# Kernel tuning notes

Measured on AMD Instinct MI355X. Metric: run time of the kernel, lower is better.

The kernel has to match this reference:

```python
import jax, jax.numpy as jnp
import numpy as np

B, N, FEAT, D = 8, 2048, 64, 6
RADIUS, NSAMPLE, TOPK, NHEAD, NLAYER = 0.3, 64, 16, 8, 2
EPS = 1e-5


def _bn(x, p, axis=1):
    # eval-mode batchnorm; p rows = (gamma, beta, running_mean, running_var)
    g, b, m, v = p
    sh = [1] * x.ndim
    sh[axis] = -1
    rs = lambda t: t.reshape(sh)
    return (x - rs(m)) * (rs(g) / jnp.sqrt(rs(v) + EPS)) + rs(b)


def _ln(x, g, b):
    mu = jnp.mean(x, -1, keepdims=True)
    var = jnp.mean((x - mu) ** 2, -1, keepdims=True)
    return (x - mu) / jnp.sqrt(var + EPS) * g + b


def _mha(x, w_in, b_in, w_out, b_out):
    bsz, n, e = x.shape
    hd = e // NHEAD
    qkv = x @ w_in.T + b_in                      # [B,N,3E]
    q, k, v = jnp.split(qkv, 3, axis=-1)
    sp = lambda t: t.reshape(bsz, n, NHEAD, hd).transpose(0, 2, 1, 3)  # [B,H,N,hd]
    q, k, v = sp(q), sp(k), sp(v)
    att = jax.nn.softmax(jnp.einsum('bhnd,bhmd->bhnm', q, k) * (1.0 / hd ** 0.5), axis=-1)
    o = jnp.einsum('bhnm,bhmd->bhnd', att, v).transpose(0, 2, 1, 3).reshape(bsz, n, e)
    return o @ w_out.T + b_out


def _forward(sortvec, input, tl_win, tl_bin, tl_wout, tl_bout, tl_w1, tl_b1, tl_w2, tl_b2,
             tl_ln1g, tl_ln1b, tl_ln2g, tl_ln2b,
             fg_w0, fg_b0, fg_w1, fg_b1, fg_w2, fg_b2, fbn0, fbn1, fbn2,
             rc_w0, rc_b0, rc_w1, rc_b1, rc_w2, rc_b2, rbn0, rbn1, rbn2,
             fl_w0, fl_b0, fl_w1, fl_b1, lbn0, lbn1):
    b = sortvec.shape[0]
    n = sortvec.shape[-1]
    relu = jax.nn.relu

    # --- input self-attention (2 post-norm TransformerEncoder layers) ---
    x = sortvec[:, 0].transpose(0, 2, 1)         # [B,N,FEAT]
    for l in range(NLAYER):
        a = _mha(x, tl_win[l], tl_bin[l], tl_wout[l], tl_bout[l])
        x = _ln(x + a, tl_ln1g[l], tl_ln1b[l])
        f = relu(x @ tl_w1[l].T + tl_b1[l]) @ tl_w2[l].T + tl_b2[l]
        x = _ln(x + f, tl_ln2g[l], tl_ln2b[l])

    # --- feat_generator (RFFNet: Conv2d(FEAT,1) then 1x1 convs) + BN + relu ---
    s = jnp.einsum('cf,bnf->bcn', fg_w0, x) + fg_b0[:, None]   # [B,64,N]
    s = relu(_bn(s, fbn0))
    s = relu(_bn(jnp.einsum('co,bon->bcn', fg_w1, s) + fg_b1[:, None], fbn1))
    s = relu(_bn(jnp.einsum('co,bon->bcn', fg_w2, s) + fg_b2[:, None], fbn2))
    scores = s[:, 0]                              # [B,N]

    # --- top-k point selection ---
    _, idx = jax.lax.top_k(scores, TOPK)          # [B,K]
    all_points = input.transpose(0, 2, 1)         # [B,N,6]
    bidx = jnp.arange(b)[:, None]
    query = all_points[bidx, idx]                 # [B,K,6]

    # --- query_ball_point (PointNet++ style) ---
    xyz, qxyz = all_points[..., :3], query[..., :3]
    sqr = jnp.sum((qxyz[:, :, None, :] - xyz[:, None, :, :]) ** 2, -1)   # [B,K,N]
    gidx = jnp.where(sqr > RADIUS ** 2, n, jnp.arange(n)[None, None, :])
    gidx = jnp.sort(gidx, axis=-1)[..., :NSAMPLE]                        # [B,K,S]
    gidx = jnp.where(gidx == n, gidx[..., :1], gidx)
    radius_points = all_points[jnp.arange(b)[:, None, None], gidx]       # [B,K,S,6]
    grouped = jnp.concatenate([query[:, :, None, :], radius_points], axis=2)  # [B,K,S+1,6]

    # --- radius_cnn (Conv3d (1,S+1,6) then 1x1x1) + BN3d + relu ---
    r = jnp.einsum('cpd,bkpd->bck', rc_w0, grouped) + rc_b0[:, None]     # [B,128,K]
    r = relu(_bn(r, rbn0))
    r = relu(_bn(jnp.einsum('co,bok->bck', rc_w1, r) + rc_b1[:, None], rbn1))
    r = relu(_bn(jnp.einsum('co,bok->bck', rc_w2, r) + rc_b2[:, None], rbn2))  # [B,512,K]

    # --- flatten + Linear/BN1d/relu chain ---
    h = r.reshape(b, -1)                          # [B, 512*K]
    h = relu(_bn(h @ fl_w0.T + fl_b0, lbn0))
    h = relu(_bn(h @ fl_w1.T + fl_b1, lbn1))
    return h[..., None], idx                      # [B,512,1], [B,K]


def setup_inputs() -> dict:
    key = jax.random.key(0)
    ks = iter(jax.random.split(key, 80))
    rnd = lambda shape, s=0.02: jax.random.normal(next(ks), shape, jnp.float32) * s

    def bn_p(c):
        g = 1.0 + rnd((c,))
        bb = rnd((c,))
        m = rnd((c,))
        v = 1.0 + 0.1 * jnp.abs(rnd((c,), 1.0))
        return jnp.stack([g, bb, m, v])

    F = FEAT
    return dict(
        sortvec=jax.random.normal(next(ks), (B, 1, F, N), jnp.float32),
        input=jax.random.normal(next(ks), (B, D, N), jnp.float32),
        tl_win=rnd((NLAYER, 3 * F, F)), tl_bin=rnd((NLAYER, 3 * F)),
        tl_wout=rnd((NLAYER, F, F)), tl_bout=rnd((NLAYER, F)),
        tl_w1=rnd((NLAYER, 2048, F)), tl_b1=rnd((NLAYER, 2048)),
        tl_w2=rnd((NLAYER, F, 2048)), tl_b2=rnd((NLAYER, F)),
        tl_ln1g=jnp.ones((NLAYER, F)), tl_ln1b=jnp.zeros((NLAYER, F)),
        tl_ln2g=jnp.ones((NLAYER, F)), tl_ln2b=jnp.zeros((NLAYER, F)),
        fg_w0=rnd((64, F), 0.1), fg_b0=jnp.zeros((64,)),
        fg_w1=rnd((16, 64), 0.1), fg_b1=jnp.zeros((16,)),
        fg_w2=rnd((1, 16), 0.1), fg_b2=jnp.zeros((1,)),
        fbn0=bn_p(64), fbn1=bn_p(16), fbn2=bn_p(1),
        rc_w0=rnd((128, NSAMPLE + 1, D), 0.05), rc_b0=jnp.zeros((128,)),
        rc_w1=rnd((256, 128), 0.05), rc_b1=jnp.zeros((256,)),
        rc_w2=rnd((512, 256), 0.05), rc_b2=jnp.zeros((512,)),
        rbn0=bn_p(128), rbn1=bn_p(256), rbn2=bn_p(512),
        fl_w0=rnd((1024, 512 * TOPK), 0.02), fl_b0=jnp.zeros((1024,)),
        fl_w1=rnd((512, 1024), 0.02), fl_b1=jnp.zeros((512,)),
        lbn0=bn_p(1024), lbn1=bn_p(512),
    )


def reference(sortvec, input, tl_win, tl_bin, tl_wout, tl_bout, tl_w1, tl_b1, tl_w2, tl_b2,
              tl_ln1g, tl_ln1b, tl_ln2g, tl_ln2b,
              fg_w0, fg_b0, fg_w1, fg_b1, fg_w2, fg_b2, fbn0, fbn1, fbn2,
              rc_w0, rc_b0, rc_w1, rc_b1, rc_w2, rc_b2, rbn0, rbn1, rbn2,
              fl_w0, fl_b0, fl_w1, fl_b1, lbn0, lbn1):
    return _forward(sortvec, input, tl_win, tl_bin, tl_wout, tl_bout, tl_w1, tl_b1, tl_w2, tl_b2,
                    tl_ln1g, tl_ln1b, tl_ln2g, tl_ln2b,
                    fg_w0, fg_b0, fg_w1, fg_b1, fg_w2, fg_b2, fbn0, fbn1, fbn2,
                    rc_w0, rc_b0, rc_w1, rc_b1, rc_w2, rc_b2, rbn0, rbn1, rbn2,
                    fl_w0, fl_b0, fl_w1, fl_b1, lbn0, lbn1)
```

## Files before the change

kernel.cpp:

```cpp
#include <hip/hip_runtime.h>
#include <hip/hip_bf16.h>
#include <math.h>

#define BB 8
#define NN 2048
#define FF 64
#define DD 6
#define NSAMP 64
#define TOPK 16
#define NHEAD 8
#define HD 8
#define NLAYER 2
#define EPSF 1e-5f
#define R2 0.09f

typedef short short8 __attribute__((ext_vector_type(8)));
typedef float f32x4 __attribute__((ext_vector_type(4)));
typedef unsigned uint4v __attribute__((ext_vector_type(4)));
typedef unsigned int u32;

__device__ inline unsigned pk2(float x) {
  unsigned b = __float_as_uint(x);
  unsigned hi = (b + 0x7fffu + ((b >> 16) & 1u)) >> 16;
  float r = x - __uint_as_float(hi << 16);
  unsigned c = __float_as_uint(r);
  unsigned lo = (c + 0x7fffu + ((c >> 16) & 1u)) >> 16;
  return (hi << 16) | lo;
}

__device__ inline unsigned short bf16r(float x) {
  unsigned b = __float_as_uint(x);
  return (unsigned short)((b + 0x7fffu + ((b >> 16) & 1u)) >> 16);
}

__device__ __forceinline__ void gl16(const void* g, void* l) {
  __builtin_amdgcn_global_load_lds((const __attribute__((address_space(1))) u32*)g,
                                   (__attribute__((address_space(3))) u32*)l, 16, 0, 0);
}

__global__ void k_transpose(const float* __restrict__ sv, float* __restrict__ x) {
  int i = blockIdx.x * 256 + threadIdx.x;
  if (i >= BB * NN * FF) return;
  int f = i % FF;
  int n = (i / FF) % NN;
  int b = i / (FF * NN);
  x[i] = sv[(b * FF + f) * NN + n];
}

__global__ void k_wimg(const float* __restrict__ w1, const float* __restrict__ w2,
                       unsigned short* __restrict__ img) {
  int i = blockIdx.x * 256 + threadIdx.x;
  int e = i & 4095;
  int plane = (i >> 12) & 3;
  int chg = (i >> 14) & 31;
  int l = i >> 19;
  int r = e >> 6, sh = (e >> 3) & 7, inner = e & 7;
  int s = sh ^ (r & 7);
  float v;
  if (plane < 2) v = w1[((size_t)(l * 2048 + chg * 64 + r)) * 64 + s * 8 + inner];
  else           v = w2[((size_t)(l * 64 + r)) * 2048 + chg * 64 + s * 8 + inner];
  unsigned p = pk2(v);
  img[i] = (unsigned short)((plane & 1) ? (p & 0xffffu) : (p >> 16));
}

__global__ void k_qkv3(const float* __restrict__ x, const float* __restrict__ win,
                       const float* __restrict__ bin, float* __restrict__ qbuf,
                       uint4* __restrict__ kp4, uint4* __restrict__ vp4) {
  __shared__ float xs[64 * 68];
  __shared__ float ws[64 * 68];
  int row0 = blockIdx.x * 64, y = blockIdx.y, col0 = y * 64;
  int t = threadIdx.x;
  #pragma unroll
  for (int i = 0; i < 4; ++i) {
    int q = t + i * 256, r = q >> 4, c = (q & 15) * 4;
    *(float4*)(xs + r * 68 + c) = *(const float4*)(x + (size_t)(row0 + r) * 64 + c);
    *(float4*)(ws + r * 68 + c) = *(const float4*)(win + (size_t)(col0 + r) * 64 + c);
  }
  __syncthreads();
  int tx = t & 15, ty = t >> 4;
  float acc[4][4] = {};
  for (int f = 0; f < 64; f += 4) {
    float4 xv[4], wv[4];
    #pragma unroll
    for (int ri = 0; ri < 4; ++ri) xv[ri] = *(const float4*)(xs + (ty * 4 + ri) * 68 + f);
    #pragma unroll
    for (int ci = 0; ci < 4; ++ci) wv[ci] = *(const float4*)(ws + (tx + 16 * ci) * 68 + f);
    #pragma unroll
    for (int ri = 0; ri < 4; ++ri)
      #pragma unroll
      for (int ci = 0; ci < 4; ++ci)
        acc[ri][ci] += xv[ri].x * wv[ci].x + xv[ri].y * wv[ci].y +
                       xv[ri].z * wv[ci].z + xv[ri].w * wv[ci].w;
  }
  int b = row0 >> 11, n0 = row0 & (NN - 1);
  if (y == 0) {
    #pragma unroll
    for (int ri = 0; ri < 4; ++ri)
      #pragma unroll
      for (int ci = 0; ci < 4; ++ci) {
        int r = row0 + ty * 4 + ri, c = tx + 16 * ci;
        qbuf[(size_t)r * 64 + c] = acc[ri][ci] + bin[c];
      }
    return;
  }
  __syncthreads();
  unsigned short* l16 = (unsigned short*)xs;
  if (y == 1) {
    #pragma unroll
    for (int ri = 0; ri < 4; ++ri)
      #pragma unroll
      for (int ci = 0; ci < 4; ++ci) {
        int r = ty * 4 + ri, c = tx + 16 * ci;
        l16[r * 72 + c] = bf16r(acc[ri][ci] + bin[64 + c]);
      }
    __syncthreads();
    #pragma unroll
    for (int i = 0; i < 2; ++i) {
      int idx = t + i * 256;
      int h = idx >> 6, tok = idx & 63;
      uint4 v = *(const uint4*)(l16 + tok * 72 + h * 8);
      kp4[(size_t)(b * NHEAD + h) * NN + n0 + tok] = v;
    }
  } else {
    #pragma unroll
    for (int ri = 0; ri < 4; ++ri)
      #pragma unroll
      for (int ci = 0; ci < 4; ++ci) {
        int r = ty * 4 + ri, c = tx + 16 * ci;
        l16[c * 72 + r] = bf16r(acc[ri][ci] + bin[128 + c]);
      }
    __syncthreads();
    #pragma unroll
    for (int i = 0; i < 2; ++i) {
      int idx = t + i * 256;
      int c = idx >> 3, seg = idx & 7;
      uint4 v = *(const uint4*)(l16 + c * 72 + seg * 8);
      vp4[(size_t)(b * 64 + c) * (NN / 8) + (n0 >> 3) + seg] = v;
    }
  }
}

__global__ void __launch_bounds__(256, 8)
k_attn8(const float* __restrict__ q, const uint4* __restrict__ kp4,
        const unsigned* __restrict__ vp32, float* __restrict__ a) {
  __shared__ uint4 kb4[256];
  __shared__ __attribute__((aligned(16))) unsigned short vb16[9 * 264];
  int t = threadIdx.x;
  int lane = t & 63, w = t >> 6;
  int nIdx = lane & 15, lq = lane >> 4;
  int h = blockIdx.y, b = blockIdx.z;
  int qwb = blockIdx.x * 64 + w * 16;
  int bh = b * NHEAD + h;
  const float kf = 0.35355339059327373f * 1.4426950408889634f;
  short8 qF = {0, 0, 0, 0, 0, 0, 0, 0};
  if (lq == 0) {
    const float* qr = q + ((size_t)(b * NN + qwb + nIdx)) * 64 + h * HD;
    #pragma unroll
    for (int j = 0; j < 8; ++j) qF[j] = (short)bf16r(qr[j] * kf);
  }
  f32x4 acc = {0.f, 0.f, 0.f, 0.f};
  const uint4* kbase = kp4 + (size_t)bh * NN;
  const unsigned* vbase = vp32 + (size_t)bh * HD * (NN / 2);
  int vn = nIdx < 9 ? nIdx : 8;
  int voff = ((lq & 1) << 4) + ((lq >> 1) << 3);
  if (t < 132) ((unsigned*)(vb16 + 8 * 264))[t] = 0x3f803f80u;
  uint4 kreg = kbase[t];
  unsigned vreg[4];
  #pragma unroll
  for (int i = 0; i < 4; ++i) {
    int g = t + i * 256;
    vreg[i] = vbase[(g >> 7) * (NN / 2) + (g & 127)];
  }
  for (int kc = 0; kc < NN; kc += 256) {
    __syncthreads();
    kb4[t] = kreg;
    #pragma unroll
    for (int i = 0; i < 4; ++i) {
      int g = t + i * 256;
      ((unsigned*)vb16)[(g >> 7) * 132 + (g & 127)] = vreg[i];
    }
    __syncthreads();
    if (kc + 256 < NN) {
      kreg = kbase[kc + 256 + t];
      #pragma unroll
      for (int i = 0; i < 4; ++i) {
        int g = t + i * 256;
        vreg[i] = vbase[(g >> 7) * (NN / 2) + ((kc + 256) >> 1) + (g & 127)];
      }
    }
    for (int s = 0; s < 8; ++s) {
      int kb = s * 32;
      unsigned pk_[4];
      #pragma unroll
      for (int half = 0; half < 2; ++half) {
        int key = kb + half * 16 + nIdx;
        short8 aK = {0, 0, 0, 0, 0, 0, 0, 0};
        if (lq == 0) aK = *(const short8*)(kb4 + key);
        f32x4 c = {0.f, 0.f, 0.f, 0.f};
        c = __builtin_amdgcn_mfma_f32_16x16x32_bf16(aK, qF, c, 0, 0, 0);
        unsigned u0 = __float_as_uint(__builtin_amdgcn_exp2f(c[0]));
        unsigned u1 = __float_as_uint(__builtin_amdgcn_exp2f(c[1]));
        unsigned u2 = __float_as_uint(__builtin_amdgcn_exp2f(c[2]));
        unsigned u3 = __float_as_uint(__builtin_amdgcn_exp2f(c[3]));
        pk_[half * 2]     = (u0 >> 16) | (u1 & 0xffff0000u);
        pk_[half * 2 + 1] = (u2 >> 16) | (u3 & 0xffff0000u);
      }
      unsigned e0 = (unsigned)__shfl_xor((int)pk_[0], 16);
      unsigned e1 = (unsigned)__shfl_xor((int)pk_[1], 16);
      unsigned e2 = (unsigned)__shfl_xor((int)pk_[2], 16);
      unsigned e3 = (unsigned)__shfl_xor((int)pk_[3], 16);
      bool odd = (lq & 1);
      uint4v bw;
      bw[0] = odd ? e2 : pk_[0];
      bw[1] = odd ? e3 : pk_[1];
      bw[2] = odd ? pk_[2] : e0;
      bw[3] = odd ? pk_[3] : e1;
      short8 bP = *(short8*)&bw;
      short8 aV = *(const short8*)(vb16 + vn * 264 + kb + voff);
      acc = __builtin_amdgcn_mfma_f32_16x16x32_bf16(aV, bP, acc, 0, 0, 0);
    }
  }
  float lr = __shfl(acc[0], 32 + nIdx);
  if (lq < 2) {
    int row = qwb + nIdx;
    float4 o;
    o.x = acc[0] / lr; o.y = acc[1] / lr; o.z = acc[2] / lr; o.w = acc[3] / lr;
    *(float4*)(a + ((size_t)(b * NN + row)) * 64 + h * HD + lq * 4) = o;
  }
}

__global__ void k_proj2(const float* __restrict__ a, const float* __restrict__ wout,
                        const float* __restrict__ bout, const float* __restrict__ g,
                        const float* __restrict__ be, float* __restrict__ x) {
  __shared__ float xs[64 * 68];
  __shared__ float ws[64 * 68];
  int row0 = blockIdx.x * 64;
  int t = threadIdx.x;
  #pragma unroll
  for (int i = 0; i < 4; ++i) {
    int q = t + i * 256, r = q >> 4, c = (q & 15) * 4;
    *(float4*)(xs + r * 68 + c) = *(const float4*)(a + (size_t)(row0 + r) * 64 + c);
    *(float4*)(ws + r * 68 + c) = *(const float4*)(wout + r * 64 + c);
  }
  __syncthreads();
  int tx = t & 15, ty = t >> 4;
  float acc[4][4] = {};
  for (int f = 0; f < 64; f += 4) {
    float4 xv[4], wv[4];
    #pragma unroll
    for (int ri = 0; ri < 4; ++ri) xv[ri] = *(const float4*)(xs + (ty * 4 + ri) * 68 + f);
    #pragma unroll
    for (int ci = 0; ci < 4; ++ci) wv[ci] = *(const float4*)(ws + (tx + 16 * ci) * 68 + f);
    #pragma unroll
    for (int ri = 0; ri < 4; ++ri)
      #pragma unroll
      for (int ci = 0; ci < 4; ++ci)
        acc[ri][ci] += xv[ri].x * wv[ci].x + xv[ri].y * wv[ci].y +
                       xv[ri].z * wv[ci].z + xv[ri].w * wv[ci].w;
  }
  #pragma unroll
  for (int ri = 0; ri < 4; ++ri) {
    int rl = ty * 4 + ri;
    float val[4], s = 0.f, sq = 0.f;
    #pragma unroll
    for (int ci = 0; ci < 4; ++ci) {
      int c = tx + 16 * ci;
      val[ci] = x[(size_t)(row0 + rl) * 64 + c] + bout[c] + acc[ri][ci];
      s += val[ci]; sq += val[ci] * val[ci];
    }
    #pragma unroll
    for (int off = 1; off < 16; off <<= 1) { s += __shfl_xor(s, off); sq += __shfl_xor(sq, off); }
    float mean = s * (1.f / 64.f);
    float var = sq * (1.f / 64.f) - mean * mean;
    float rstd = rsqrtf(var + EPSF);
    #pragma unroll
    for (int ci = 0; ci < 4; ++ci) {
      int c = tx + 16 * ci;
      x[(size_t)(row0 + rl) * 64 + c] = (val[ci] - mean) * rstd * g[c] + be[c];
    }
  }
}

__global__ void __launch_bounds__(256, 2)
k_ffn7(const float* __restrict__ x, const char* __restrict__ img,
       const float* __restrict__ b1, float* __restrict__ part) {
  __shared__ __attribute__((aligned(16))) char W1b[2][16384];
  __shared__ __attribute__((aligned(16))) char W2b[16384];
  __shared__ __attribute__((aligned(16))) unsigned short hpl[2][128 * 64];
  int row0 = blockIdx.x * 128;
  int ks = blockIdx.y, kc = ks * 512;
  int t = threadIdx.x, lane = t & 63, wv = t >> 6;
  int lm = lane & 15, lq = lane >> 4;
  const char* ibase = img + (size_t)ks * 8 * 32768;

  short8 axh[2][2], axl[2][2];
  #pragma unroll
  for (int m = 0; m < 2; ++m)
    #pragma unroll
    for (int kbi = 0; kbi < 2; ++kbi) {
      const float* xr = x + (size_t)(row0 + m * 64 + wv * 16 + lm) * 64 + kbi * 32 + lq * 8;
      #pragma unroll
      for (int j = 0; j < 8; ++j) {
        unsigned p = pk2(xr[j]);
        axh[m][kbi][j] = (short)(p >> 16);
        axl[m][kbi][j] = (short)(p & 0xffffu);
      }
    }
  float bv[8][4];
  #pragma unroll
  for (int ch = 0; ch < 8; ++ch)
    #pragma unroll
    for (int tn = 0; tn < 4; ++tn)
      bv[ch][tn] = b1[kc + ch * 64 + tn * 16 + lm];
  asm volatile("s_waitcnt vmcnt(0)" ::: "memory");
  __builtin_amdgcn_sched_barrier(0);
  #pragma unroll
  for (int i = 0; i < 4; ++i)
    gl16(ibase + i * 4096 + t * 16, &W1b[0][i * 4096 + t * 16]);

  f32x4 acc[2][4];
  #pragma unroll
  for (int m = 0; m < 2; ++m)
    #pragma unroll
    for (int tn = 0; tn < 4; ++tn) acc[m][tn] = (f32x4){0.f, 0.f, 0.f, 0.f};

  #pragma unroll
  for (int ch = 0; ch < 8; ++ch) {
    const int p = ch & 1;
    const char* cbase = ibase + ch * 32768;
    #pragma unroll
    for (int i = 0; i < 4; ++i)
      gl16(cbase + 16384 + i * 4096 + t * 16, &W2b[i * 4096 + t * 16]);
    if (ch < 7) {
      #pragma unroll
      for (int i = 0; i < 4; ++i)
        gl16(cbase + 32768 + i * 4096 + t * 16, &W1b[p ^ 1][i * 4096 + t * 16]);
    }
    if (ch < 7) { asm volatile("s_waitcnt vmcnt(8)" ::: "memory"); }
    else        { asm volatile("s_waitcnt vmcnt(4)" ::: "memory"); }
    __builtin_amdgcn_sched_barrier(0);
    __builtin_amdgcn_s_barrier();
    __builtin_amdgcn_sched_barrier(0);
    const char* P0h = W1b[p];
    const char* P0l = W1b[p] + 8192;
    f32x4 h4[2][4];
    #pragma unroll
    for (int m = 0; m < 2; ++m)
      #pragma unroll
      for (int tn = 0; tn < 4; ++tn) h4[m][tn] = (f32x4){0.f, 0.f, 0.f, 0.f};
    #pragma unroll
    for (int kbi = 0; kbi < 2; ++kbi) {
      int sw = (((kbi * 4 + lq) ^ (lm & 7)) << 4);
      #pragma unroll
      for (int tn = 0; tn < 4; ++tn) {
        int brow = tn * 16 + lm;
        short8 bhi = *(const short8*)(P0h + brow * 128 + sw);
        short8 blo = *(const short8*)(P0l + brow * 128 + sw);
        #pragma unroll
        for (int m = 0; m < 2; ++m) {
          h4[m][tn] = __builtin_amdgcn_mfma_f32_16x16x32_bf16(axh[m][kbi], bhi, h4[m][tn], 0, 0, 0);
          h4[m][tn] = __builtin_amdgcn_mfma_f32_16x16x32_bf16(axh[m][kbi], blo, h4[m][tn], 0, 0, 0);
          h4[m][tn] = __builtin_amdgcn_mfma_f32_16x16x32_bf16(axl[m][kbi], bhi, h4[m][tn], 0, 0, 0);
        }
      }
    }
    #pragma unroll
    for (int m = 0; m < 2; ++m)
      #pragma unroll
      for (int tn = 0; tn < 4; ++tn)
        #pragma unroll
        for (int r = 0; r < 4; ++r) {
          float hv = fmaxf(h4[m][tn][r] + bv[ch][tn], 0.f);
          unsigned u = __float_as_uint(hv);
          float resid = hv - __uint_as_float(u & 0xffff0000u);
          unsigned c2 = __float_as_uint(resid);
          int hrow = m * 64 + wv * 16 + lq * 4 + r, hcol = tn * 16 + lm;
          int off = hrow * 128 + (((hcol >> 3) ^ (hrow & 7)) << 4) + ((hcol & 7) << 1);
          *(unsigned short*)((char*)hpl[0] + off) = (unsigned short)(u >> 16);
          *(unsigned short*)((char*)hpl[1] + off) =
              (unsigned short)((c2 + 0x7fffu + ((c2 >> 16) & 1u)) >> 16);
        }
    if (ch < 7) { asm volatile("s_waitcnt vmcnt(4)" ::: "memory"); }
    else        { asm volatile("s_waitcnt vmcnt(0)" ::: "memory"); }
    __builtin_amdgcn_sched_barrier(0);
    __builtin_amdgcn_s_barrier();
    __builtin_amdgcn_sched_barrier(0);
    const char* P1h = W2b;
    const char* P1l = W2b + 8192;
    #pragma unroll
    for (int kbi = 0; kbi < 2; ++kbi) {
      short8 a2h[2], a2l[2];
      #pragma unroll
      for (int m = 0; m < 2; ++m) {
        int arow = m * 64 + wv * 16 + lm;
        int swa = (((kbi * 4 + lq) ^ (arow & 7)) << 4);
        a2h[m] = *(const short8*)((const char*)hpl[0] + arow * 128 + swa);
        a2l[m] = *(const short8*)((const char*)hpl[1] + arow * 128 + swa);
      }
      int swb = (((kbi * 4 + lq) ^ (lm & 7)) << 4);
      #pragma unroll
      for (int tn = 0; tn < 4; ++tn) {
        int brow = tn * 16 + lm;
        short8 bhi = *(const short8*)(P1h + brow * 128 + swb);
        short8 blo = *(const short8*)(P1l + brow * 128 + swb);
        #pragma unroll
        for (int m = 0; m < 2; ++m) {
          acc[m][tn] = __builtin_amdgcn_mfma_f32_16x16x32_bf16(a2h[m], bhi, acc[m][tn], 0, 0, 0);
          acc[m][tn] = __builtin_amdgcn_mfma_f32_16x16x32_bf16(a2h[m], blo, acc[m][tn], 0, 0, 0);
          acc[m][tn] = __builtin_amdgcn_mfma_f32_16x16x32_bf16(a2l[m], bhi, acc[m][tn], 0, 0, 0);
        }
      }
    }
    __builtin_amdgcn_s_barrier();
    __builtin_amdgcn_sched_barrier(0);
  }
  float* fb = (float*)hpl;
  #pragma unroll
  for (int m = 0; m < 2; ++m)
    #pragma unroll
    for (int tn = 0; tn < 4; ++tn)
      #pragma unroll
      for (int r = 0; r < 4; ++r) {
        int row = m * 64 + wv * 16 + lq * 4 + r;
        int col = (tn * 16 + lm) ^ ((row & 7) << 2);
        fb[row * 64 + col] = acc[m][tn][r];
      }
  __syncthreads();
  float* pb = part + (size_t)ks * (BB * NN * 64);
  #pragma unroll
  for (int i = 0; i < 8; ++i) {
    int idx = t * 4 + i * 1024;
    int row = idx >> 6, c0 = idx & 63;
    int c0s = c0 ^ ((row & 7) << 2);
    float4 v = *(const float4*)(fb + row * 64 + c0s);
    *(float4*)(pb + (size_t)(row0 + row) * 64 + c0) = v;
  }
}

__global__ void k_ffn_ln(const float* __restrict__ part, const float* __restrict__ b2,
                         const float* __restrict__ g, const float* __restrict__ be,
                         float* __restrict__ x) {
  int row = blockIdx.x * 4 + (threadIdx.x >> 6);
  int j = threadIdx.x & 63;
  size_t o = (size_t)row * 64 + j;
  const size_t S = (size_t)BB * NN * 64;
  float val = x[o] + b2[j] + ((part[o] + part[o + S]) + (part[o + 2 * S] + part[o + 3 * S]));
  float s = val;
  for (int off = 32; off; off >>= 1) s += __shfl_xor(s, off);
  s *= (1.f / 64.f);
  float d = val - s;
  float v = d * d;
  for (int off = 32; off; off >>= 1) v += __shfl_xor(v, off);
  v *= (1.f / 64.f);
  x[o] = d * rsqrtf(v + EPSF) * g[j] + be[j];
}

__global__ void k_fg2(const float* __restrict__ x,
                      const float* __restrict__ w0, const float* __restrict__ b0, const float* __restrict__ bn0,
                      const float* __restrict__ w1, const float* __restrict__ b1, const float* __restrict__ bn1,
                      const float* __restrict__ w2, const float* __restrict__ b2, const float* __restrict__ bn2,
                      float* __restrict__ scores) {
  __shared__ float xs[64 * 68];
  __shared__ float ws[64 * 68];
  __shared__ float s0s[64 * 68];
  __shared__ float s1s[64 * 20];
  int row0 = blockIdx.x * 64;
  int t = threadIdx.x;
  #pragma unroll
  for (int i = 0; i < 4; ++i) {
    int q = t + i * 256, r = q >> 4, c = (q & 15) * 4;
    *(float4*)(xs + r * 68 + c) = *(const float4*)(x + (size_t)(row0 + r) * 64 + c);
    *(float4*)(ws + r * 68 + c) = *(const float4*)(w0 + r * 64 + c);
  }
  __syncthreads();
  int tx = t & 15, ty = t >> 4;
  float acc[4][4] = {};
  for (int f = 0; f < 64; f += 4) {
    float4 xv[4], wv[4];
    #pragma unroll
    for (int ri = 0; ri < 4; ++ri) xv[ri] = *(const float4*)(xs + (ty * 4 + ri) * 68 + f);
    #pragma unroll
    for (int ci = 0; ci < 4; ++ci) wv[ci] = *(const float4*)(ws + (tx + 16 * ci) * 68 + f);
    #pragma unroll
    for (int ri = 0; ri < 4; ++ri)
      #pragma unroll
      for (int ci = 0; ci < 4; ++ci)
        acc[ri][ci] += xv[ri].x * wv[ci].x + xv[ri].y * wv[ci].y +
                       xv[ri].z * wv[ci].z + xv[ri].w * wv[ci].w;
  }
  #pragma unroll
  for (int ri = 0; ri < 4; ++ri)
    #pragma unroll
    for (int ci = 0; ci < 4; ++ci) {
      int c = tx + 16 * ci;
      float sc = bn0[c] * rsqrtf(bn0[192 + c] + EPSF);
      float v = (acc[ri][ci] + b0[c] - bn0[128 + c]) * sc + bn0[64 + c];
      s0s[(ty * 4 + ri) * 68 + c] = fmaxf(v, 0.f);
    }
  __syncthreads();
  {
    int rl = t & 63, j0 = t >> 6;
    #pragma unroll
    for (int i = 0; i < 4; ++i) {
      int j = j0 + 4 * i;
      float s = b1[j];
      const float* wr = w1 + j * 64;
      #pragma unroll 16
      for (int c = 0; c < 64; ++c) s += s0s[rl * 68 + c] * wr[c];
      float sc = bn1[j] * rsqrtf(bn1[48 + j] + EPSF);
      s = (s - bn1[32 + j]) * sc + bn1[16 + j];
      s1s[rl * 20 + j] = fmaxf(s, 0.f);
    }
  }
  __syncthreads();
  if (t < 64) {
    float s = b2[0];
    #pragma unroll
    for (int o = 0; o < 16; ++o) s += s1s[t * 20 + o] * w2[o];
    float sc = bn2[0] * rsqrtf(bn2[3] + EPSF);
    s = (s - bn2[2]) * sc + bn2[1];
    scores[row0 + t] = fmaxf(s, 0.f);
  }
}

__global__ void k_topk2(const float* __restrict__ scores, int* __restrict__ idx,
                        float* __restrict__ out_idx) {
  int b = blockIdx.x, t = threadIdx.x;
  float v[8];
  int base = b * NN;
  #pragma unroll
  for (int u = 0; u < 8; ++u) v[u] = scores[base + t + 256 * u];
  __shared__ float wvs[4];
  __shared__ int wis[4];
  __shared__ int winner;
  unsigned taken = 0;
  for (int r = 0; r < TOPK; ++r) {
    float best = -1e30f; int bi = 1 << 30;
    #pragma unroll
    for (int u = 0; u < 8; ++u) {
      if (!((taken >> u) & 1)) {
        float vv = v[u]; int ii = t + 256 * u;
        if (vv > best || (vv == best && ii < bi)) { best = vv; bi = ii; }
      }
    }
    for (int off = 32; off; off >>= 1) {
      float ov = __shfl_xor(best, off);
      int oi = __shfl_xor(bi, off);
      if (ov > best || (ov == best && oi < bi)) { best = ov; bi = oi; }
    }
    if ((t & 63) == 0) { wvs[t >> 6] = best; wis[t >> 6] = bi; }
    __syncthreads();
    if (t == 0) {
      float B = wvs[0]; int I = wis[0];
      #pragma unroll
      for (int q = 1; q < 4; ++q)
        if (wvs[q] > B || (wvs[q] == B && wis[q] < I)) { B = wvs[q]; I = wis[q]; }
      winner = I;
      idx[b * TOPK + r] = I;
      out_idx[b * TOPK + r] = (float)I;
    }
    __syncthreads();
    int w = winner;
    if ((w & 255) == t) taken |= 1u << (w >> 8);
  }
}

__global__ void __launch_bounds__(512)
k_group(const float* __restrict__ inp, const int* __restrict__ idx,
        const float* __restrict__ w0, const float* __restrict__ b0, const float* __restrict__ bn0,
        const float* __restrict__ w1, const float* __restrict__ b1, const float* __restrict__ bn1,
        const float* __restrict__ w2, const float* __restrict__ b2, const float* __restrict__ bn2,
        float* __restrict__ r2g) {
  __shared__ int swave[8 * 64];
  __shared__ int scnt[8];
  __shared__ int gidx[NSAMP];
  __shared__ __attribute__((aligned(16))) float gsh[65 * DD];
  __shared__ __attribute__((aligned(16))) float r0[128];
  __shared__ __attribute__((aligned(16))) float r1[256];
  int k = blockIdx.x, b = blockIdx.y;
  int t = threadIdx.x;
  int lane = t & 63, w = t >> 6;
  int qn = idx[b * TOPK + k];
  const float* px = inp + (size_t)b * DD * NN;
  float qx = px[qn], qy = px[NN + qn], qz = px[2 * NN + qn];
  {
    int cnt = 0;
    #pragma unroll
    for (int i = 0; i < 4; ++i) {
      int n = w * 256 + i * 64 + lane;
      float dx = px[n] - qx, dy = px[NN + n] - qy, dz = px[2 * NN + n] - qz;
      bool flag = (dx * dx + dy * dy + dz * dz <= R2);
      unsigned long long m = __ballot(flag);
      int pos = cnt + __popcll(m & ((1ull << lane) - 1ull));
      if (flag && pos < NSAMP) swave[w * 64 + pos] = n;
      cnt += (int)__popcll(m);
    }
    if (lane == 0) scnt[w] = cnt < NSAMP ? cnt : NSAMP;
  }
  __syncthreads();
  if (t < NSAMP) {
    int run = 0, val = -1;
    #pragma unroll
    for (int ww = 0; ww < 8; ++ww) {
      int c = scnt[ww];
      int loc = t - run;
      if (loc >= 0 && loc < c) val = swave[ww * 64 + loc];
      run += c;
    }
    gidx[t] = val;
  }
  __syncthreads();
  if (t < NSAMP) {
    int g0 = gidx[0];
    int gt = gidx[t];
    gidx[t] = (gt < 0) ? g0 : gt;
  }
  __syncthreads();
  if (t < 65 * DD) {
    int p = t / DD, d = t - p * DD;
    int n = (p == 0) ? qn : gidx[p - 1];
    gsh[t] = px[d * NN + n];
  }
  __syncthreads();
  {
    int c = t >> 2, part = t & 3;
    const float2* wr = (const float2*)(w0 + c * 390 + part * 98);
    const float2* gr = (const float2*)(gsh + part * 98);
    int n2 = (part == 3) ? 48 : 49;
    float s = 0.f;
    #pragma unroll 7
    for (int i = 0; i < n2; ++i) {
      float2 a = gr[i], ww = wr[i];
      s += a.x * ww.x + a.y * ww.y;
    }
    s += __shfl_xor(s, 1);
    s += __shfl_xor(s, 2);
    if (part == 0) {
      s += b0[c];
      float sc = bn0[c] * rsqrtf(bn0[384 + c] + EPSF);
      s = (s - bn0[256 + c]) * sc + bn0[128 + c];
      r0[c] = fmaxf(s, 0.f);
    }
  }
  __syncthreads();
  {
    int c = t >> 1, part = t & 1;
    const float4* wr = (const float4*)(w1 + c * 128 + part * 64);
    const float4* rr = (const float4*)(r0 + part * 64);
    float s0 = 0.f, s1 = 0.f, s2 = 0.f, s3 = 0.f;
    #pragma unroll 8
    for (int o = 0; o < 16; ++o) {
      float4 a = rr[o], ww = wr[o];
      s0 += a.x * ww.x; s1 += a.y * ww.y; s2 += a.z * ww.z; s3 += a.w * ww.w;
    }
    float s = (s0 + s1) + (s2 + s3);
    s += __shfl_xor(s, 1);
    if (part == 0) {
      s += b1[c];
      float sc = bn1[c] * rsqrtf(bn1[768 + c] + EPSF);
      s = (s - bn1[512 + c]) * sc + bn1[256 + c];
      r1[c] = fmaxf(s, 0.f);
    }
  }
  __syncthreads();
  {
    int c = t;
    const float4* wr = (const float4*)(w2 + c * 256);
    const float4* rr = (const float4*)r1;
    float s0 = 0.f, s1 = 0.f, s2 = 0.f, s3 = 0.f;
    #pragma unroll 8
    for (int o = 0; o < 64; ++o) {
      float4 a = rr[o], ww = wr[o];
      s0 += a.x * ww.x; s1 += a.y * ww.y; s2 += a.z * ww.z; s3 += a.w * ww.w;
    }
    float s = (s0 + s1) + (s2 + s3) + b2[c];
    float sc = bn2[c] * rsqrtf(bn2[1536 + c] + EPSF);
    s = (s - bn2[1024 + c]) * sc + bn2[512 + c];
    r2g[b * 8192 + c * TOPK + k] = fmaxf(s, 0.f);
  }
}

__global__ void k_fl(const float* __restrict__ hin, const float* __restrict__ w,
                     const float* __restrict__ bias, const float* __restrict__ bn,
                     float* __restrict__ hout, int IN, int OUT) {
  int blk = blockIdx.x;
  int b = blk / OUT, j = blk % OUT;
  int lane = threadIdx.x;
  const float* hr = hin + (size_t)b * IN;
  const float* wr = w + (size_t)j * IN;
  float s = 0.f;
  for (int i = lane; i < IN; i += 64) s += hr[i] * wr[i];
  for (int o = 32; o; o >>= 1) s += __shfl_xor(s, o);
  if (lane == 0) {
    s += bias[j];
    float sc = bn[j] * rsqrtf(bn[3 * OUT + j] + EPSF);
    s = (s - bn[2 * OUT + j]) * sc + bn[OUT + j];
    hout[b * OUT + j] = fmaxf(s, 0.f);
  }
}

extern "C" void kernel_launch(void* const* d_in, const int* in_sizes, int n_in,
                              void* d_out, int out_size, void* d_ws, size_t ws_size,
                              hipStream_t stream) {
  const float* sv      = (const float*)d_in[0];
  const float* inp     = (const float*)d_in[1];
  const float* tl_win  = (const float*)d_in[2];
  const float* tl_bin  = (const float*)d_in[3];
  const float* tl_wout = (const float*)d_in[4];
  const float* tl_bout = (const float*)d_in[5];
  const float* tl_w1   = (const float*)d_in[6];
  const float* tl_b1   = (const float*)d_in[7];
  const float* tl_w2   = (const float*)d_in[8];
  const float* tl_b2   = (const float*)d_in[9];
  const float* tl_ln1g = (const float*)d_in[10];
  const float* tl_ln1b = (const float*)d_in[11];
  const float* tl_ln2g = (const float*)d_in[12];
  const float* tl_ln2b = (const float*)d_in[13];
  const float* fg_w0   = (const float*)d_in[14];
  const float* fg_b0   = (const float*)d_in[15];
  const float* fg_w1   = (const float*)d_in[16];
  const float* fg_b1   = (const float*)d_in[17];
  const float* fg_w2   = (const float*)d_in[18];
  const float* fg_b2   = (const float*)d_in[19];
  const float* fbn0    = (const float*)d_in[20];
  const float* fbn1    = (const float*)d_in[21];
  const float* fbn2    = (const float*)d_in[22];
  const float* rc_w0   = (const float*)d_in[23];
  const float* rc_b0   = (const float*)d_in[24];
  const float* rc_w1   = (const float*)d_in[25];
  const float* rc_b1   = (const float*)d_in[26];
  const float* rc_w2   = (const float*)d_in[27];
  const float* rc_b2   = (const float*)d_in[28];
  const float* rbn0    = (const float*)d_in[29];
  const float* rbn1    = (const float*)d_in[30];
  const float* rbn2    = (const float*)d_in[31];
  const float* fl_w0   = (const float*)d_in[32];
  const float* fl_b0   = (const float*)d_in[33];
  const float* fl_w1   = (const float*)d_in[34];
  const float* fl_b1   = (const float*)d_in[35];
  const float* lbn0    = (const float*)d_in[36];
  const float* lbn1    = (const float*)d_in[37];
  (void)in_sizes; (void)n_in; (void)out_size; (void)ws_size;

  float* wsp = (float*)d_ws;
  float* x      = wsp;
  float* qkv    = x + BB * NN * FF;
  float* a      = qkv + BB * NN * 192;
  float* scores = a + BB * NN * FF;
  int*   idxb   = (int*)(scores + BB * NN);
  float* r2g    = (float*)(idxb + BB * TOPK);
  float* h1g    = r2g + BB * 8192;
  unsigned short* img = (unsigned short*)(h1g + BB * 1024);
  float* qbuf = qkv;
  unsigned short* kp = (unsigned short*)(qkv + BB * NN * FF);
  unsigned short* vp = kp + (size_t)BB * NHEAD * NN * HD;
  float* part = qkv;

  float* out = (float*)d_out;

  k_transpose<<<(BB * NN * FF) / 256, 256, 0, stream>>>(sv, x);
  k_wimg<<<(NLAYER * 32 * 4 * 4096) / 256, 256, 0, stream>>>(tl_w1, tl_w2, img);

  for (int l = 0; l < NLAYER; ++l) {
    k_qkv3<<<dim3(BB * NN / 64, 3), 256, 0, stream>>>(x, tl_win + l * 192 * FF,
                                                      tl_bin + l * 192, qbuf,
                                                      (uint4*)kp, (uint4*)vp);
    k_attn8<<<dim3(NN / 64, NHEAD, BB), 256, 0, stream>>>(qbuf, (const uint4*)kp,
                                                          (const unsigned*)vp, a);
    k_proj2<<<BB * NN / 64, 256, 0, stream>>>(a, tl_wout + l * FF * FF, tl_bout + l * FF,
                                              tl_ln1g + l * FF, tl_ln1b + l * FF, x);
    k_ffn7<<<dim3(BB * NN / 128, 4), 256, 0, stream>>>(x, (const char*)(img + (size_t)l * 524288),
                                                       tl_b1 + l * 2048, part);
    k_ffn_ln<<<BB * NN / 4, 256, 0, stream>>>(part, tl_b2 + l * FF,
                                              tl_ln2g + l * FF, tl_ln2b + l * FF, x);
  }

  k_fg2<<<BB * NN / 64, 256, 0, stream>>>(x, fg_w0, fg_b0, fbn0, fg_w1, fg_b1, fbn1,
                                          fg_w2, fg_b2, fbn2, scores);
  k_topk2<<<BB, 256, 0, stream>>>(scores, idxb, out + BB * 512);
  k_group<<<dim3(TOPK, BB), 512, 0, stream>>>(inp, idxb, rc_w0, rc_b0, rbn0,
                                              rc_w1, rc_b1, rbn1, rc_w2, rc_b2, rbn2, r2g);
  k_fl<<<BB * 1024, 64, 0, stream>>>(r2g, fl_w0, fl_b0, lbn0, h1g, 8192, 1024);
  k_fl<<<BB * 512, 64, 0, stream>>>(h1g, fl_w1, fl_b1, lbn1, out, 1024, 512);
}
```

Baseline: 469.3 us.

## Batch-tile first FC layer with split-K partials and separate BN epilogue

Replaces the per-(batch,output) dot-product kernel for the 8192->1024 FC layer with a split-K kernel. Each block stages all 8 batch rows of an activation chunk in shared memory and reads each weight row once for all batches. A small second kernel sums the 8 K-partials and applies bias, batchnorm and ReLU. This removes the 8x redundant streaming of the 32 MB weight matrix, at the cost of an extra launch and a partial-sum buffer reused from existing scratch.

```diff
diff --git a/kernel.cpp b/kernel.cpp
--- a/kernel.cpp
+++ b/kernel.cpp
@@ -678,6 +678,56 @@
     s = (s - bn2[1024 + c]) * sc + bn2[512 + c];
     r2g[b * 8192 + c * TOPK + k] = fmaxf(s, 0.f);
   }
+}
+
+__global__ void __launch_bounds__(256)
+k_fl2(const float* __restrict__ hin, const float* __restrict__ w,
+      float* __restrict__ part) {
+  __shared__ float hs[8 * 1032];
+  int j0 = blockIdx.x * 16;
+  int kc = blockIdx.y * 1024;
+  int t = threadIdx.x;
+  int jj = t >> 4, l = t & 15;
+  #pragma unroll
+  for (int i = 0; i < 8; ++i) {
+    int idx = t + i * 256;
+    int b = idx >> 8, off = (idx & 255) * 4;
+    *(float4*)(hs + b * 1032 + off) = *(const float4*)(hin + (size_t)b * 8192 + kc + off);
+  }
+  __syncthreads();
+  const float* wr = w + (size_t)(j0 + jj) * 8192 + kc;
+  float acc[8] = {};
+  #pragma unroll
+  for (int k = 0; k < 16; ++k) {
+    float4 wv = *(const float4*)(wr + l * 4 + k * 64);
+    #pragma unroll
+    for (int b = 0; b < 8; ++b) {
+      float4 hv = *(const float4*)(hs + b * 1032 + l * 4 + k * 64);
+      acc[b] += wv.x * hv.x + wv.y * hv.y + wv.z * hv.z + wv.w * hv.w;
+    }
+  }
+  #pragma unroll
+  for (int b = 0; b < 8; ++b) {
+    #pragma unroll
+    for (int off = 1; off < 16; off <<= 1) acc[b] += __shfl_xor(acc[b], off);
+  }
+  if (l == 0) {
+    #pragma unroll
+    for (int b = 0; b < 8; ++b)
+      part[((size_t)blockIdx.y * 8 + b) * 1024 + j0 + jj] = acc[b];
+  }
+}
+
+__global__ void k_flc(const float* __restrict__ part, const float* __restrict__ bias,
+                      const float* __restrict__ bn, float* __restrict__ hout) {
+  int i = blockIdx.x * 256 + threadIdx.x;
+  int b = i >> 10, j = i & 1023;
+  float s = bias[j];
+  #pragma unroll
+  for (int ks = 0; ks < 8; ++ks) s += part[((size_t)ks * 8 + b) * 1024 + j];
+  float sc = bn[j] * rsqrtf(bn[3 * 1024 + j] + EPSF);
+  s = (s - bn[2 * 1024 + j]) * sc + bn[1024 + j];
+  hout[i] = fmaxf(s, 0.f);
 }
 
 __global__ void k_fl(const float* __restrict__ hin, const float* __restrict__ w,
@@ -780,6 +830,7 @@
   k_topk2<<<BB, 256, 0, stream>>>(scores, idxb, out + BB * 512);
   k_group<<<dim3(TOPK, BB), 512, 0, stream>>>(inp, idxb, rc_w0, rc_b0, rbn0,
                                               rc_w1, rc_b1, rbn1, rc_w2, rc_b2, rbn2, r2g);
-  k_fl<<<BB * 1024, 64, 0, stream>>>(r2g, fl_w0, fl_b0, lbn0, h1g, 8192, 1024);
+  k_fl2<<<dim3(64, 8), 256, 0, stream>>>(r2g, fl_w0, part);
+  k_flc<<<32, 256, 0, stream>>>(part, fl_b0, lbn0, h1g);
   k_fl<<<BB * 512, 64, 0, stream>>>(h1g, fl_w1, fl_b1, lbn1, out, 1024, 512);
 }
```

Measured after the change: 447.8 us. -4.6%, faster.
